# Kernel tuning notes

Measured on AMD Instinct MI355X. Metric: run time of the kernel, lower is better.

Reference implementation:

```python
import jax, jax.numpy as jnp
import numpy as np

# CTC-CRF constants (bonito defaults): state_len=5, alphabet='NACGT' -> n_base=4
STATE_LEN = 5
N_BASE = 4
S = N_BASE ** STATE_LEN          # 1024 states
NZ = N_BASE + 1                  # 5 incoming transitions per state (stay + 4 moves)
C = S * NZ                       # 5120 score channels per timestep


def _make_idx():
    # idx[s] = indices into alpha (previous states) feeding state s.
    # Matches torch: cat([arange(S)[:,None], arange(S).repeat_interleave(n_base).reshape(n_base,-1).T], 1)
    a = np.arange(S)
    idx = np.concatenate([a[:, None], np.repeat(a, N_BASE).reshape(N_BASE, S).T], axis=1)
    return jnp.asarray(idx, dtype=jnp.int32)  # [S, NZ]


def setup_inputs() -> dict:
    key = jax.random.key(0)
    T, N = 2000, 32
    scores = jax.random.normal(key, (T, N, C), dtype=jnp.float32)
    return {"scores": scores}


def reference(scores) -> jnp.ndarray:
    # Faithful jax version of CTC_CRF.logZ(scores) with the Log semiring:
    #   alpha[t+1] = logsumexp(Ms[t] + alpha[t][:, idx], axis=-1)
    #   logZ = logsumexp(alpha[T] + vT, axis=1)
    T, N, _ = scores.shape
    idx = _make_idx()                      # [S, NZ] int32
    Ms = scores.reshape(T, N, S, NZ)       # [T, N, S, NZ]
    v0 = jnp.zeros((N, S), dtype=scores.dtype)  # semiring one = 0.0
    vT = jnp.zeros((N, S), dtype=scores.dtype)

    def step(alpha, Ms_t):
        # alpha: [N, S]; gather predecessors -> [N, S, NZ]; semiring mul = add; sum = logsumexp
        a_next = jax.nn.logsumexp(Ms_t + alpha[:, idx], axis=-1)
        return a_next, None

    alpha_T, _ = jax.lax.scan(step, v0, Ms)
    return jax.nn.logsumexp(alpha_T + vT, axis=1)  # [N]
```

## Files before the change

### kernel.cpp

```cpp
#include <hip/hip_runtime.h>
#include <cstdint>
#include <cstddef>


#define NB 32
#define SD 1024
#define CD 5120

typedef float f4a __attribute__((ext_vector_type(4), aligned(4)));

__device__ __forceinline__ float fexp2(float x) { return __builtin_amdgcn_exp2f(x); }
__device__ __forceinline__ float flog2(float x) { return __builtin_amdgcn_logf(x); }

__global__ void __launch_bounds__(1024) ctc_logz(const float* __restrict__ scores,
                                                 float* __restrict__ out, int T) {
  __shared__ float ap[2 * SD];
  __shared__ float red[16];

  const int tid = threadIdx.x;
  const int n = blockIdx.x;
  const int lane = tid & 63;
  const int wid = tid >> 6;
  const int p4 = (tid >> 2) << 2;
  const int awr = ((tid & 255) << 2) | (tid >> 8);

  ap[tid] = 1.f;
  ap[SD + tid] = 1.f;
  float a_cur = 1.f;
  int cacc = 0;

  const float K = 1.44269504088896340736f;
  const float LN2 = 0.69314718055994530942f;

  const float* sn = scores + (size_t)n * CD + (size_t)tid * 5;
  const size_t tstr = (size_t)NB * CD;
  const size_t str8 = 8 * tstr;

  auto CP = [&](int t, const f4a& qa, float qb) {
    const int rbuf = ((t + 1) & 1) * SD;
    const f4a av = *(const f4a*)&ap[rbuf + p4];
    const float R = ap[rbuf];
    const int xb = (__float_as_int(R) >> 23) & 0xFF;
    cacc += xb;
    const float nLf = (float)(127 - xb);
    float e0 = fexp2(__builtin_fmaf(qa.x, K, nLf));
    float e1 = fexp2(__builtin_fmaf(qa.y, K, nLf));
    float e2 = fexp2(__builtin_fmaf(qa.z, K, nLf));
    float e3 = fexp2(__builtin_fmaf(qa.w, K, nLf));
    float e4 = fexp2(__builtin_fmaf(qb,   K, nLf));
    float s = e0 * a_cur;
    s = __builtin_fmaf(e1, av.x, s);
    s = __builtin_fmaf(e2, av.y, s);
    s = __builtin_fmaf(e3, av.z, s);
    s = __builtin_fmaf(e4, av.w, s);
    a_cur = s;
    ap[(t & 1) * SD + awr] = s;
    asm volatile("s_waitcnt lgkmcnt(0)\n\ts_barrier" ::: "memory");
  };

#define PRO(c)                                                              \
  const float* P##c = sn + (size_t)((c) < T ? (c) : T - 1) * tstr;          \
  f4a qa##c = *(const f4a*)P##c;                                            \
  float qb##c = P##c[4];                                                    \
  P##c += str8;
  PRO(0) PRO(1) PRO(2) PRO(3) PRO(4) PRO(5) PRO(6) PRO(7)
#undef PRO

  __syncthreads();

#define RL(c)                                                               \
  qa##c = *(const f4a*)P##c;                                                \
  qb##c = P##c[4];                                                          \
  P##c += str8;

  int t = 0;
  for (; t + 16 <= T; t += 8) {
    CP(t + 0, qa0, qb0); RL(0)
    CP(t + 1, qa1, qb1); RL(1)
    CP(t + 2, qa2, qb2); RL(2)
    CP(t + 3, qa3, qb3); RL(3)
    CP(t + 4, qa4, qb4); RL(4)
    CP(t + 5, qa5, qb5); RL(5)
    CP(t + 6, qa6, qb6); RL(6)
    CP(t + 7, qa7, qb7); RL(7)
  }
#undef RL

#define EPI1(c)                                                             \
  if (t + (c) < T) {                                                        \
    CP(t + (c), qa##c, qb##c);                                              \
    if (t + 8 + (c) < T) { qa##c = *(const f4a*)P##c; qb##c = P##c[4]; }    \
  }
  EPI1(0) EPI1(1) EPI1(2) EPI1(3) EPI1(4) EPI1(5) EPI1(6) EPI1(7)
#undef EPI1
  t += 8;
#define EPI2(c) if (t + (c) < T) CP(t + (c), qa##c, qb##c);
  EPI2(0) EPI2(1) EPI2(2) EPI2(3) EPI2(4) EPI2(5) EPI2(6) EPI2(7)
#undef EPI2

  float v = a_cur;
#pragma unroll
  for (int d = 1; d < 64; d <<= 1) v += __shfl_xor(v, d, 64);
  if (lane == 0) red[wid] = v;
  __syncthreads();
  if (tid == 0) {
    float ssum = red[0];
#pragma unroll
    for (int i = 1; i < 16; ++i) ssum += red[i];
    out[n] = LN2 * ((float)(cacc - 127 * T) + flog2(ssum));
  }
}

extern "C" void kernel_launch(void* const* d_in, const int* in_sizes, int n_in,
                              void* d_out, int out_size, void* d_ws, size_t ws_size,
                              hipStream_t stream) {
  const float* scores = (const float*)d_in[0];
  float* out = (float*)d_out;
  const long long tot = (long long)in_sizes[0];
  const int T = (int)(tot / ((long long)NB * CD));
  ctc_logz<<<dim3(NB), dim3(1024), 0, stream>>>(scores, out, T);
}
```

Before: 761.8 us.

## Compute two CRF states per thread with 512-thread blocks

Halves the block size so each thread computes two adjacent states per timestep. The two states share the same four predecessor loads from LDS, and the results are written as a single float2 store. This reduces barrier participants and LDS read traffic, and prefetch depth drops from 8 to 4 timesteps to fit the wider per-thread loads. The cost is more serial exp work per thread and less latency hiding for the global score loads.

```diff
diff --git a/kernel.cpp b/kernel.cpp
--- a/kernel.cpp
+++ b/kernel.cpp
@@ -6,107 +6,112 @@
 #define NB 32
 #define SD 1024
 #define CD 5120
+#define NT 512
 
 typedef float f4a __attribute__((ext_vector_type(4), aligned(4)));
+typedef float f2a __attribute__((ext_vector_type(2), aligned(8)));
 
 __device__ __forceinline__ float fexp2(float x) { return __builtin_amdgcn_exp2f(x); }
 __device__ __forceinline__ float flog2(float x) { return __builtin_amdgcn_logf(x); }
 
-__global__ void __launch_bounds__(1024) ctc_logz(const float* __restrict__ scores,
-                                                 float* __restrict__ out, int T) {
+__global__ void __launch_bounds__(NT) ctc_logz(const float* __restrict__ scores,
+                                               float* __restrict__ out, int T) {
   __shared__ float ap[2 * SD];
-  __shared__ float red[16];
+  __shared__ float red[8];
 
-  const int tid = threadIdx.x;
+  const int u = threadIdx.x;
   const int n = blockIdx.x;
-  const int lane = tid & 63;
-  const int wid = tid >> 6;
-  const int p4 = (tid >> 2) << 2;
-  const int awr = ((tid & 255) << 2) | (tid >> 8);
+  const int lane = u & 63;
+  const int wid = u >> 6;
+  const int pb = u >> 1;
 
-  ap[tid] = 1.f;
-  ap[SD + tid] = 1.f;
-  float a_cur = 1.f;
+  ap[u] = 1.f; ap[u + 512] = 1.f; ap[u + 1024] = 1.f; ap[u + 1536] = 1.f;
+  float a0 = 1.f, a1 = 1.f;
   int cacc = 0;
 
   const float K = 1.44269504088896340736f;
   const float LN2 = 0.69314718055994530942f;
 
-  const float* sn = scores + (size_t)n * CD + (size_t)tid * 5;
+  const float* sn = scores + (size_t)n * CD + (size_t)u * 10;
   const size_t tstr = (size_t)NB * CD;
-  const size_t str8 = 8 * tstr;
+  const size_t str4 = 4 * tstr;
 
-  auto CP = [&](int t, const f4a& qa, float qb) {
-    const int rbuf = ((t + 1) & 1) * SD;
-    const f4a av = *(const f4a*)&ap[rbuf + p4];
-    const float R = ap[rbuf];
+  auto CP = [&](int t, const f4a& qa, const f4a& qb, const f2a& qc) {
+    const int rb = ((t + 1) & 1) * SD;
+    const float R = ap[rb];
     const int xb = (__float_as_int(R) >> 23) & 0xFF;
     cacc += xb;
     const float nLf = (float)(127 - xb);
-    float e0 = fexp2(__builtin_fmaf(qa.x, K, nLf));
-    float e1 = fexp2(__builtin_fmaf(qa.y, K, nLf));
-    float e2 = fexp2(__builtin_fmaf(qa.z, K, nLf));
-    float e3 = fexp2(__builtin_fmaf(qa.w, K, nLf));
-    float e4 = fexp2(__builtin_fmaf(qb,   K, nLf));
-    float s = e0 * a_cur;
-    s = __builtin_fmaf(e1, av.x, s);
-    s = __builtin_fmaf(e2, av.y, s);
-    s = __builtin_fmaf(e3, av.z, s);
-    s = __builtin_fmaf(e4, av.w, s);
-    a_cur = s;
-    ap[(t & 1) * SD + awr] = s;
+    const float p0 = ap[rb + pb];
+    const float p1 = ap[rb + pb + 256];
+    const float p2 = ap[rb + pb + 512];
+    const float p3 = ap[rb + pb + 768];
+    float s0 = fexp2(__builtin_fmaf(qa.x, K, nLf)) * a0;
+    s0 = __builtin_fmaf(fexp2(__builtin_fmaf(qa.y, K, nLf)), p0, s0);
+    s0 = __builtin_fmaf(fexp2(__builtin_fmaf(qa.z, K, nLf)), p1, s0);
+    s0 = __builtin_fmaf(fexp2(__builtin_fmaf(qa.w, K, nLf)), p2, s0);
+    s0 = __builtin_fmaf(fexp2(__builtin_fmaf(qb.x, K, nLf)), p3, s0);
+    float s1 = fexp2(__builtin_fmaf(qb.y, K, nLf)) * a1;
+    s1 = __builtin_fmaf(fexp2(__builtin_fmaf(qb.z, K, nLf)), p0, s1);
+    s1 = __builtin_fmaf(fexp2(__builtin_fmaf(qb.w, K, nLf)), p1, s1);
+    s1 = __builtin_fmaf(fexp2(__builtin_fmaf(qc.x, K, nLf)), p2, s1);
+    s1 = __builtin_fmaf(fexp2(__builtin_fmaf(qc.y, K, nLf)), p3, s1);
+    a0 = s0; a1 = s1;
+    f2a w; w.x = s0; w.y = s1;
+    *(f2a*)&ap[(t & 1) * SD + (u << 1)] = w;
     asm volatile("s_waitcnt lgkmcnt(0)\n\ts_barrier" ::: "memory");
   };
 
 #define PRO(c)                                                              \
   const float* P##c = sn + (size_t)((c) < T ? (c) : T - 1) * tstr;          \
   f4a qa##c = *(const f4a*)P##c;                                            \
-  float qb##c = P##c[4];                                                    \
-  P##c += str8;
-  PRO(0) PRO(1) PRO(2) PRO(3) PRO(4) PRO(5) PRO(6) PRO(7)
+  f4a qb##c = *(const f4a*)(P##c + 4);                                      \
+  f2a qc##c = *(const f2a*)(P##c + 8);                                      \
+  P##c += str4;
+  PRO(0) PRO(1) PRO(2) PRO(3)
 #undef PRO
 
   __syncthreads();
 
 #define RL(c)                                                               \
   qa##c = *(const f4a*)P##c;                                                \
-  qb##c = P##c[4];                                                          \
-  P##c += str8;
+  qb##c = *(const f4a*)(P##c + 4);                                          \
+  qc##c = *(const f2a*)(P##c + 8);                                          \
+  P##c += str4;
 
   int t = 0;
-  for (; t + 16 <= T; t += 8) {
-    CP(t + 0, qa0, qb0); RL(0)
-    CP(t + 1, qa1, qb1); RL(1)
-    CP(t + 2, qa2, qb2); RL(2)
-    CP(t + 3, qa3, qb3); RL(3)
-    CP(t + 4, qa4, qb4); RL(4)
-    CP(t + 5, qa5, qb5); RL(5)
-    CP(t + 6, qa6, qb6); RL(6)
-    CP(t + 7, qa7, qb7); RL(7)
+  for (; t + 8 <= T; t += 4) {
+    CP(t + 0, qa0, qb0, qc0); RL(0)
+    CP(t + 1, qa1, qb1, qc1); RL(1)
+    CP(t + 2, qa2, qb2, qc2); RL(2)
+    CP(t + 3, qa3, qb3, qc3); RL(3)
   }
 #undef RL
 
 #define EPI1(c)                                                             \
   if (t + (c) < T) {                                                        \
-    CP(t + (c), qa##c, qb##c);                                              \
-    if (t + 8 + (c) < T) { qa##c = *(const f4a*)P##c; qb##c = P##c[4]; }    \
+    CP(t + (c), qa##c, qb##c, qc##c);                                       \
+    if (t + 4 + (c) < T) {                                                  \
+      qa##c = *(const f4a*)P##c; qb##c = *(const f4a*)(P##c + 4);           \
+      qc##c = *(const f2a*)(P##c + 8);                                      \
+    }                                                                       \
   }
-  EPI1(0) EPI1(1) EPI1(2) EPI1(3) EPI1(4) EPI1(5) EPI1(6) EPI1(7)
+  EPI1(0) EPI1(1) EPI1(2) EPI1(3)
 #undef EPI1
-  t += 8;
-#define EPI2(c) if (t + (c) < T) CP(t + (c), qa##c, qb##c);
-  EPI2(0) EPI2(1) EPI2(2) EPI2(3) EPI2(4) EPI2(5) EPI2(6) EPI2(7)
+  t += 4;
+#define EPI2(c) if (t + (c) < T) CP(t + (c), qa##c, qb##c, qc##c);
+  EPI2(0) EPI2(1) EPI2(2) EPI2(3)
 #undef EPI2
 
-  float v = a_cur;
+  float v = a0 + a1;
 #pragma unroll
   for (int d = 1; d < 64; d <<= 1) v += __shfl_xor(v, d, 64);
   if (lane == 0) red[wid] = v;
   __syncthreads();
-  if (tid == 0) {
+  if (u == 0) {
     float ssum = red[0];
 #pragma unroll
-    for (int i = 1; i < 16; ++i) ssum += red[i];
+    for (int i = 1; i < 8; ++i) ssum += red[i];
     out[n] = LN2 * ((float)(cacc - 127 * T) + flog2(ssum));
   }
 }
@@ -118,5 +123,5 @@
   float* out = (float*)d_out;
   const long long tot = (long long)in_sizes[0];
   const int T = (int)(tot / ((long long)NB * CD));
-  ctc_logz<<<dim3(NB), dim3(1024), 0, stream>>>(scores, out, T);
+  ctc_logz<<<dim3(NB), dim3(NT), 0, stream>>>(scores, out, T);
 }
```

After: 1.146 ms. 1.5x slower.

## Use swizzled scalar LDS reads with DPP broadcast and deferred damped rescale

Applied to the files above, without the earlier changes.

Each lane now loads a single swizzled float from LDS instead of a float4 of predecessors. The four predecessor values are broadcast within each quad using DPP quad_perm, and XOR swizzles on the read and write offsets are meant to avoid bank conflicts. The renormalisation exponent is taken from the previous step's reference value, scaled down by a factor of four and applied one step later, so the exponent extract and convert leave the critical path between load and compute. Prefetch depth drops from 8 timesteps to 4, which lowers register pressure but hides less global-load latency. The damped, lagged scaling could allow more growth in magnitude and risks overflow or underflow on other inputs.

```diff
diff --git a/kernel.cpp b/kernel.cpp
--- a/kernel.cpp
+++ b/kernel.cpp
@@ -12,90 +12,98 @@
 __device__ __forceinline__ float fexp2(float x) { return __builtin_amdgcn_exp2f(x); }
 __device__ __forceinline__ float flog2(float x) { return __builtin_amdgcn_logf(x); }
 
+template <int CTRL>
+__device__ __forceinline__ float dppq(float v) {
+  return __int_as_float(
+      __builtin_amdgcn_update_dpp(0, __float_as_int(v), CTRL, 0xF, 0xF, true));
+}
+
 __global__ void __launch_bounds__(1024) ctc_logz(const float* __restrict__ scores,
                                                  float* __restrict__ out, int T) {
   __shared__ float ap[2 * SD];
   __shared__ float red[16];
 
-  const int tid = threadIdx.x;
+  const int u = threadIdx.x;
   const int n = blockIdx.x;
-  const int lane = tid & 63;
-  const int wid = tid >> 6;
-  const int p4 = (tid >> 2) << 2;
-  const int awr = ((tid & 255) << 2) | (tid >> 8);
+  const int lane = u & 63;
+  const int wid = u >> 6;
+  const int p = u >> 2, c = u & 3;
+  const int rdoff = (c << 8) | (p ^ (c << 3));
+  const int wroff = u ^ ((u & 0x300) >> 5);
 
-  ap[tid] = 1.f;
-  ap[SD + tid] = 1.f;
+  ap[u] = 1.f; ap[SD + u] = 1.f;
   float a_cur = 1.f;
-  int cacc = 0;
+  float nLf = 0.f;
+  int Lnext = 0, cacc = 0;
 
   const float K = 1.44269504088896340736f;
   const float LN2 = 0.69314718055994530942f;
 
-  const float* sn = scores + (size_t)n * CD + (size_t)tid * 5;
+  const float* sn = scores + (size_t)n * CD + (size_t)u * 5;
   const size_t tstr = (size_t)NB * CD;
-  const size_t str8 = 8 * tstr;
+  const size_t str4 = 4 * tstr;
 
   auto CP = [&](int t, const f4a& qa, float qb) {
-    const int rbuf = ((t + 1) & 1) * SD;
-    const f4a av = *(const f4a*)&ap[rbuf + p4];
-    const float R = ap[rbuf];
-    const int xb = (__float_as_int(R) >> 23) & 0xFF;
-    cacc += xb;
-    const float nLf = (float)(127 - xb);
+    const int rb = ((t + 1) & 1) * SD;
+    const float vr = ap[rb + rdoff];
+    const float R = ap[rb];
+    const float p0 = dppq<0x00>(vr);
+    const float p1 = dppq<0x55>(vr);
+    const float p2 = dppq<0xAA>(vr);
+    const float p3 = dppq<0xFF>(vr);
     float e0 = fexp2(__builtin_fmaf(qa.x, K, nLf));
     float e1 = fexp2(__builtin_fmaf(qa.y, K, nLf));
     float e2 = fexp2(__builtin_fmaf(qa.z, K, nLf));
     float e3 = fexp2(__builtin_fmaf(qa.w, K, nLf));
     float e4 = fexp2(__builtin_fmaf(qb,   K, nLf));
     float s = e0 * a_cur;
-    s = __builtin_fmaf(e1, av.x, s);
-    s = __builtin_fmaf(e2, av.y, s);
-    s = __builtin_fmaf(e3, av.z, s);
-    s = __builtin_fmaf(e4, av.w, s);
+    s = __builtin_fmaf(e1, p0, s);
+    s = __builtin_fmaf(e2, p1, s);
+    s = __builtin_fmaf(e3, p2, s);
+    s = __builtin_fmaf(e4, p3, s);
     a_cur = s;
-    ap[(t & 1) * SD + awr] = s;
+    cacc += Lnext;
+    ap[(t & 1) * SD + wroff] = s;
+    const int xb = ((__float_as_int(R) >> 23) & 0xFF) - 127;
+    Lnext = xb >> 2;
+    nLf = (float)(-Lnext);
     asm volatile("s_waitcnt lgkmcnt(0)\n\ts_barrier" ::: "memory");
   };
 
-#define PRO(c)                                                              \
-  const float* P##c = sn + (size_t)((c) < T ? (c) : T - 1) * tstr;          \
-  f4a qa##c = *(const f4a*)P##c;                                            \
-  float qb##c = P##c[4];                                                    \
-  P##c += str8;
-  PRO(0) PRO(1) PRO(2) PRO(3) PRO(4) PRO(5) PRO(6) PRO(7)
+#define PRO(cc)                                                             \
+  const float* P##cc = sn + (size_t)((cc) < T ? (cc) : T - 1) * tstr;       \
+  f4a qa##cc = *(const f4a*)P##cc;                                          \
+  float qb##cc = P##cc[4];                                                  \
+  P##cc += str4;
+  PRO(0) PRO(1) PRO(2) PRO(3)
 #undef PRO
 
   __syncthreads();
 
-#define RL(c)                                                               \
-  qa##c = *(const f4a*)P##c;                                                \
-  qb##c = P##c[4];                                                          \
-  P##c += str8;
+#define RL(cc)                                                              \
+  qa##cc = *(const f4a*)P##cc;                                              \
+  qb##cc = P##cc[4];                                                        \
+  P##cc += str4;
 
   int t = 0;
-  for (; t + 16 <= T; t += 8) {
+  for (; t + 8 <= T; t += 4) {
     CP(t + 0, qa0, qb0); RL(0)
     CP(t + 1, qa1, qb1); RL(1)
     CP(t + 2, qa2, qb2); RL(2)
     CP(t + 3, qa3, qb3); RL(3)
-    CP(t + 4, qa4, qb4); RL(4)
-    CP(t + 5, qa5, qb5); RL(5)
-    CP(t + 6, qa6, qb6); RL(6)
-    CP(t + 7, qa7, qb7); RL(7)
   }
 #undef RL
 
-#define EPI1(c)                                                             \
-  if (t + (c) < T) {                                                        \
-    CP(t + (c), qa##c, qb##c);                                              \
-    if (t + 8 + (c) < T) { qa##c = *(const f4a*)P##c; qb##c = P##c[4]; }    \
+#define EPI1(cc)                                                            \
+  if (t + (cc) < T) {                                                       \
+    CP(t + (cc), qa##cc, qb##cc);                                           \
+    if (t + 4 + (cc) < T) { qa##cc = *(const f4a*)P##cc; qb##cc = P##cc[4]; }\
   }
-  EPI1(0) EPI1(1) EPI1(2) EPI1(3) EPI1(4) EPI1(5) EPI1(6) EPI1(7)
+  EPI1(0) EPI1(1) EPI1(2) EPI1(3)
 #undef EPI1
-  t += 8;
-#define EPI2(c) if (t + (c) < T) CP(t + (c), qa##c, qb##c);
-  EPI2(0) EPI2(1) EPI2(2) EPI2(3) EPI2(4) EPI2(5) EPI2(6) EPI2(7)
+  t += 4;
+#define EPI2(cc) if (t + (cc) < T) CP(t + (cc), qa##cc, qb##cc);
+  EPI2(0) EPI2(1) EPI2(2) EPI2(3)
 #undef EPI2
 
   float v = a_cur;
@@ -103,11 +111,11 @@
   for (int d = 1; d < 64; d <<= 1) v += __shfl_xor(v, d, 64);
   if (lane == 0) red[wid] = v;
   __syncthreads();
-  if (tid == 0) {
+  if (u == 0) {
     float ssum = red[0];
 #pragma unroll
     for (int i = 1; i < 16; ++i) ssum += red[i];
-    out[n] = LN2 * ((float)(cacc - 127 * T) + flog2(ssum));
+    out[n] = LN2 * ((float)cacc + flog2(ssum));
   }
 }
 
```

Measured after the change: 761.3 us. Within noise of the previous version (-0.1%).
